# Kernel tuning notes

Hardware: AMD Instinct MI355X
Metric: run time of the kernel (lower is better)

## Reference

```python
import jax, jax.numpy as jnp
import numpy as np

N = 100000      # nodes
E = 320000      # edges
D = 128         # num_node_in_embeddings
DE = 256        # num_edge_in_embeddings = 2*D
NOBJ = 160
NREL = 27
BN_EPS = 1e-5   # eval-mode BatchNorm with running_mean=0, running_var=1


def setup_inputs() -> dict:
    key = jax.random.key(0)
    ks = jax.random.split(key, 24)
    f32 = jnp.float32
    def rn(k, shape, scale=0.05):
        return jax.random.normal(k, shape, f32) * scale
    return {
        "node_feats": jax.random.normal(ks[0], (N, D), f32),
        "edge_index": jax.random.randint(ks[1], (E, 2), 0, N),
        # GCNConv layers (W: [in,out], bias)
        "gcn1_W": rn(ks[2], (D, D // 2)), "gcn1_b": rn(ks[3], (D // 2,)),
        "gcn2_W": rn(ks[4], (D // 2, D)), "gcn2_b": rn(ks[5], (D,)),
        # edge attention (Linear(DE, D//2))
        "eattn_W": rn(ks[6], (DE, D // 2)), "eattn_b": rn(ks[7], (D // 2,)),
        # node attention (Linear(D, DE//2)) and indicator reduction (Linear(DE, DE//2))
        "nattn_W": rn(ks[8], (D, DE // 2)), "nattn_b": rn(ks[9], (DE // 2,)),
        "nred_W": rn(ks[10], (DE, DE // 2)), "nred_b": rn(ks[11], (DE // 2,)),
        # edge MLPs (1x1 Conv1d == Linear)
        "emlp1_W": rn(ks[12], (DE, DE // 2)), "emlp1_b": rn(ks[13], (DE // 2,)),
        "emlp2_W": rn(ks[14], (DE // 2, DE)), "emlp2_b": rn(ks[15], (DE,)),
        # node classification head
        "nlin1_W": rn(ks[16], (D, D // 2)),
        "nbn_g": jnp.ones((D // 2,), f32) + rn(ks[17], (D // 2,)),
        "nbn_b": rn(ks[18], (D // 2,)),
        "nlin2_W": rn(ks[19], (D // 2, NOBJ)),
        # edge classification head
        "elin1_W": rn(ks[20], (DE, DE // 2)),
        "ebn_g": jnp.ones((DE // 2,), f32) + rn(ks[21], (DE // 2,)),
        "ebn_b": rn(ks[22], (DE // 2,)),
        "elin2_W": rn(ks[23], (DE // 2, NREL)),
    }


def _seg_mean(vals, idx, n):
    # torch_scatter 'mean': sum / clamp(count, 1)
    s = jax.ops.segment_sum(vals, idx, num_segments=n)
    c = jax.ops.segment_sum(jnp.ones((vals.shape[0], 1), vals.dtype), idx, num_segments=n)
    return s / jnp.maximum(c, 1.0)


def _gcn_conv(x, src, dst, W, b, n):
    # PyG GCNConv, add_self_loops=True, symmetric normalization.
    lin = x @ W
    deg = jax.ops.segment_sum(jnp.ones((src.shape[0],), x.dtype), dst, num_segments=n) + 1.0
    dis = jax.lax.rsqrt(deg)                       # deg^{-1/2}, includes self-loop
    norm = dis[src] * dis[dst]                     # per-edge norm
    agg = jax.ops.segment_sum(lin[src] * norm[:, None], dst, num_segments=n)
    return agg + lin * (dis * dis)[:, None] + b    # self-loop term + bias


def _bn_eval(x, g, b):
    # eval-mode BatchNorm1d with running_mean=0, running_var=1
    return x * (g / jnp.sqrt(1.0 + BN_EPS)) + b


def reference(node_feats, edge_index, gcn1_W, gcn1_b, gcn2_W, gcn2_b,
              eattn_W, eattn_b, nattn_W, nattn_b, nred_W, nred_b,
              emlp1_W, emlp1_b, emlp2_W, emlp2_b,
              nlin1_W, nbn_g, nbn_b, nlin2_W,
              elin1_W, ebn_g, ebn_b, elin2_W):
    n = node_feats.shape[0]
    src = edge_index[:, 0]
    dst = edge_index[:, 1]

    # edge feature init: [subject, object - subject]  -> [E, DE]
    subj = node_feats[src]
    edge_feats = jnp.concatenate([subj, node_feats[dst] - subj], axis=1)

    # edge attention -> scatter-mean indicators over rows/cols -> node gate
    edge_ind = edge_feats @ eattn_W + eattn_b            # [E, D/2]
    row = _seg_mean(edge_ind, src, n)                    # [N, D/2]
    col = _seg_mean(edge_ind, dst, n)                    # [N, D/2]
    agg_edge_indicator = jax.nn.sigmoid(row * col)

    # two GCN layers (dropout is identity in eval mode)
    h = jax.nn.relu(_gcn_conv(node_feats, src, dst, gcn1_W, gcn1_b, n)) * agg_edge_indicator
    h = jax.nn.relu(_gcn_conv(h, src, dst, gcn2_W, gcn2_b, n))           # [N, D]

    # node attention -> per-edge gate
    node_ind = jax.nn.relu(h @ nattn_W + nattn_b)                        # [N, DE/2]
    econcat = jnp.concatenate([node_ind[src], node_ind[dst]], axis=1)    # [E, DE]
    agg_node_indicator = jax.nn.sigmoid(econcat @ nred_W + nred_b)       # [E, DE/2]

    # edge MLPs (1x1 convs == linears over edges)
    ef = jax.nn.relu(edge_feats @ emlp1_W + emlp1_b) * agg_node_indicator
    ef = jax.nn.relu(ef @ emlp2_W + emlp2_b)                             # [E, DE]

    # node head: linear -> BN(eval) -> leaky_relu(0.2) -> linear -> softmax over classes
    nx = jax.nn.leaky_relu(_bn_eval(h @ nlin1_W, nbn_g, nbn_b), 0.2)
    node_logits = jax.nn.softmax(nx @ nlin2_W, axis=1)                   # [N, NOBJ]

    # edge head: note original applies softmax on dim=1 of [1,E,NREL] -> over EDGES
    ex = jax.nn.leaky_relu(_bn_eval(ef @ elin1_W, ebn_g, ebn_b), 0.2)
    edge_logits = jax.nn.softmax(ex @ elin2_W, axis=0)                   # [E, NREL]

    return (node_logits, edge_logits)
```

## Files before the change

kernel.cpp:

```cpp
#include <hip/hip_runtime.h>

#define NN 100000
#define EE 320000

typedef unsigned int uint32;
typedef __attribute__((ext_vector_type(8))) short bf16x8;
typedef __attribute__((ext_vector_type(4))) float f32x4;
typedef __attribute__((ext_vector_type(16))) float f32x16;

__device__ __forceinline__ float4 ld4(const float* p){ return *(const float4*)p; }
__device__ __forceinline__ void st4(float* p, const float4 v){ *(float4*)p = v; }
__device__ __forceinline__ float sigm(float x){ return 1.f/(1.f + expf(-x)); }
__device__ __forceinline__ short f2b(float f){
  union { float f; uint32 u; } v; v.f = f;
  uint32 r = (v.u + 0x7FFFu + ((v.u>>16)&1u)) >> 16;
  return (short)r;
}
__device__ __forceinline__ float b2f(short s){
  union { uint32 u; float f; } v; v.u = ((uint32)(unsigned short)s) << 16; return v.f;
}

constexpr int EM_STORE=0, EM_BRELU=1, EM_BNLK=2;

template<int K,int NOUT,int EM>
__global__ __launch_bounds__(256) void gemm_k(
    const float* __restrict__ A,
    const float* __restrict__ W, const float* __restrict__ bias,
    const float* __restrict__ bng,
    float* __restrict__ C, int M)
{
  constexpr int CN = NOUT/16;
  __shared__ float As[16][68];
  __shared__ float Ws[16][NOUT];
  const int t  = threadIdx.x;
  const int tx = t & 15, ty = t >> 4;
  const int row0 = blockIdx.x * 64;

  float acc[4][CN];
  #pragma unroll
  for (int i=0;i<4;i++)
    #pragma unroll
    for (int j=0;j<CN;j++) acc[i][j]=0.f;

  const int r_st  = t >> 2;
  const int kq_st = (t & 3) * 4;

  for (int k0=0;k0<K;k0+=16) {
    {
      float4 v = make_float4(0.f,0.f,0.f,0.f);
      const int gr = row0 + r_st;
      if (gr < M) v = ld4(A + (size_t)gr*K + k0 + kq_st);
      As[kq_st+0][r_st]=v.x; As[kq_st+1][r_st]=v.y;
      As[kq_st+2][r_st]=v.z; As[kq_st+3][r_st]=v.w;
    }
    {
      constexpr int C4 = NOUT/4;
      for (int i=t;i<16*C4;i+=256){ int kk=i/C4, c4=(i%C4)*4;
        st4(&Ws[kk][c4], ld4(W + (size_t)(k0+kk)*NOUT + c4)); }
    }
    __syncthreads();
    #pragma unroll
    for (int kk=0;kk<16;kk++){
      float a0,a1,a2,a3;
      { const float4 av = *(const float4*)&As[kk][ty*4]; a0=av.x;a1=av.y;a2=av.z;a3=av.w; }
      float b[CN];
      if constexpr ((CN & 3) == 0) {
        #pragma unroll
        for (int j4=0;j4<CN;j4+=4){
          const float4 bv = *(const float4*)&Ws[kk][tx*CN+j4];
          b[j4]=bv.x;b[j4+1]=bv.y;b[j4+2]=bv.z;b[j4+3]=bv.w; }
      } else {
        #pragma unroll
        for (int j=0;j<CN;j++) b[j]=Ws[kk][tx*CN+j];
      }
      #pragma unroll
      for (int j=0;j<CN;j++){
        acc[0][j]=fmaf(a0,b[j],acc[0][j]);
        acc[1][j]=fmaf(a1,b[j],acc[1][j]);
        acc[2][j]=fmaf(a2,b[j],acc[2][j]);
        acc[3][j]=fmaf(a3,b[j],acc[3][j]);
      }
    }
    __syncthreads();
  }

  float sc[CN], sh[CN];
  if constexpr (EM==EM_BNLK) {
    const float r_ = rsqrtf(1.f + 1e-5f);
    #pragma unroll
    for (int j=0;j<CN;j++){ int c=tx*CN+j; sc[j]=bng[c]*r_; sh[j]=bias[c]; }
  }
  #pragma unroll
  for (int i=0;i<4;i++){
    const int r  = row0 + ty*4+i;
    if (r >= M) continue;
    #pragma unroll
    for (int j=0;j<CN;j++){
      const int c = tx*CN+j;
      float v = acc[i][j];
      if constexpr (EM==EM_BRELU) v = fmaxf(v + bias[c], 0.f);
      else if constexpr (EM==EM_BNLK){ float x = fmaf(v, sc[j], sh[j]); v = (x>0.f)? x : 0.2f*x; }
      C[(size_t)r*NOUT + c] = v;
    }
  }
}

__global__ void k_hist(const int* __restrict__ eidx, int* cntS, int* cntD, int E){
  int e = blockIdx.x*256+threadIdx.x; if (e>=E) return;
  atomicAdd(&cntS[eidx[2*e]], 1);
  atomicAdd(&cntD[eidx[2*e+1]], 1);
}
__global__ void k_scan_sum(const int* __restrict__ cnt, int* bsum, int n){
  __shared__ int red[256];
  const int b=blockIdx.x, t=threadIdx.x;
  int s=0;
  for (int i=b*1024+t; i<n && i<(b+1)*1024; i+=256) s += cnt[i];
  red[t]=s; __syncthreads();
  for (int o=128;o;o>>=1){ if(t<o) red[t]+=red[t+o]; __syncthreads(); }
  if (t==0) bsum[b]=red[0];
}
__global__ void k_scan_top(int* bsum, int nb){
  __shared__ int sh[256];
  const int t=threadIdx.x;
  int v=(t<nb)?bsum[t]:0;
  sh[t]=v; __syncthreads();
  for (int o=1;o<256;o<<=1){
    int u=0; if(t>=o) u=sh[t-o];
    __syncthreads();
    sh[t]+=u;
    __syncthreads();
  }
  if (t<nb) bsum[t]=sh[t]-v;
}
__global__ void k_scan_out(const int* __restrict__ cnt, const int* __restrict__ bofs,
                           int* __restrict__ off, int n){
  __shared__ int sh[256];
  const int b=blockIdx.x, t=threadIdx.x;
  const int base=b*1024+t*4;
  int c0=0,c1=0,c2=0,c3=0;
  if(base+0<n)c0=cnt[base+0];
  if(base+1<n)c1=cnt[base+1];
  if(base+2<n)c2=cnt[base+2];
  if(base+3<n)c3=cnt[base+3];
  int s=c0+c1+c2+c3;
  sh[t]=s; __syncthreads();
  int v=s;
  for (int o=1;o<256;o<<=1){
    int u=0; if(t>=o) u=sh[t-o];
    __syncthreads();
    sh[t]+=u;
    __syncthreads();
  }
  const int tofs = sh[t]-v + bofs[b];
  if(base+0<n) off[base+0]=tofs;
  if(base+1<n) off[base+1]=tofs+c0;
  if(base+2<n) off[base+2]=tofs+c0+c1;
  if(base+3<n) off[base+3]=tofs+c0+c1+c2;
}
__global__ void k_copyoff(const int* __restrict__ off, int* __restrict__ cur, int n){
  int i=blockIdx.x*256+threadIdx.x;
  if (i<n) cur[i]=off[i];
}
__global__ void k_setend(int* offS, int* offD, int n, int E){
  if (threadIdx.x==0 && blockIdx.x==0){ offS[n]=E; offD[n]=E; }
}
__global__ void k_fill(const int* __restrict__ eidx, int* curS, int* curD,
                       int* __restrict__ csrS, int* __restrict__ csrD, int E){
  int e=blockIdx.x*256+threadIdx.x; if (e>=E) return;
  const int s=eidx[2*e], d=eidx[2*e+1];
  csrS[atomicAdd(&curS[s],1)] = d;
  csrD[atomicAdd(&curD[d],1)] = s;
}
__global__ void k_dis(const int* __restrict__ cntD, float* __restrict__ dis, int n){
  int i=blockIdx.x*256+threadIdx.x; if(i>=n)return;
  dis[i]=rsqrtf((float)cntD[i]+1.f);
}

__global__ void k_wprep(const float* __restrict__ eattnW, const float* __restrict__ gcn1W,
                        float* __restrict__ Wcat){
  int idx=blockIdx.x*256+threadIdx.x; if (idx>=128*192) return;
  int k=idx/192, c=idx-k*192;
  float v;
  if (c<64)       v = eattnW[(size_t)(128+k)*64 + c];
  else if (c<128) v = eattnW[(size_t)k*64 + (c-64)] - eattnW[(size_t)(128+k)*64 + (c-64)];
  else            v = gcn1W[(size_t)k*64 + (c-128)];
  Wcat[idx]=v;
}

template<int NC>
__global__ void k_gather(const float* __restrict__ src, int stride, int colbase,
                         const int* __restrict__ off, const int* __restrict__ csr,
                         float* __restrict__ out, int n){
  constexpr int TPN = NC/4;
  const int t=threadIdx.x;
  const int node = blockIdx.x*(256/TPN) + t/TPN; if (node>=n) return;
  const int cq = (t%TPN)*4;
  const int j1=off[node+1];
  float4 acc = make_float4(0.f,0.f,0.f,0.f);
  for (int j=off[node]; j<j1; ++j){
    const float4 v = ld4(src + (size_t)csr[j]*stride + colbase + cq);
    acc.x+=v.x; acc.y+=v.y; acc.z+=v.z; acc.w+=v.w;
  }
  st4(out + (size_t)node*NC + cq, acc);
}

__global__ void k_aei3(const float* __restrict__ TUL, const float* __restrict__ Q,
                       const float* __restrict__ S, const int* __restrict__ cntS,
                       const int* __restrict__ cntD, const float* __restrict__ bias,
                       float* __restrict__ aei, int n){
  int idx=blockIdx.x*256+threadIdx.x; if (idx>=n*16) return;
  const int i=idx>>4, cq=(idx&15)*4;
  const float cS=(float)cntS[i], cD=(float)cntD[i];
  const float iS=1.f/fmaxf(cS,1.f), iD=1.f/fmaxf(cD,1.f);
  const float* tul = TUL + (size_t)i*192;
  const float4 T4=ld4(tul+cq), U4=ld4(tul+64+cq);
  const float4 Q4=ld4(Q+(size_t)i*64+cq), S4=ld4(S+(size_t)i*64+cq), b4=ld4(bias+cq);
  float4 o;
  o.x=sigm(((cS*(U4.x+b4.x)+Q4.x)*iS) * ((cD*(T4.x+b4.x)+S4.x)*iD));
  o.y=sigm(((cS*(U4.y+b4.y)+Q4.y)*iS) * ((cD*(T4.y+b4.y)+S4.y)*iD));
  o.z=sigm(((cS*(U4.z+b4.z)+Q4.z)*iS) * ((cD*(T4.z+b4.z)+S4.z)*iD));
  o.w=sigm(((cS*(U4.w+b4.w)+Q4.w)*iS) * ((cD*(T4.w+b4.w)+S4.w)*iD));
  st4(aei + (size_t)i*64 + cq, o);
}

template<int NC, bool AEI>
__global__ void k_gcnagg(const float* __restrict__ lin, int stride, int colbase,
                         const int* __restrict__ off, const int* __restrict__ csr,
                         const float* __restrict__ dis, const float* __restrict__ aei,
                         const float* __restrict__ bias, float* __restrict__ h, int n){
  constexpr int TPN = NC/4;
  const int t=threadIdx.x;
  const int node = blockIdx.x*(256/TPN) + t/TPN; if (node>=n) return;
  const int cq = (t%TPN)*4;
  const int j1=off[node+1];
  float4 acc = make_float4(0.f,0.f,0.f,0.f);
  for (int j=off[node]; j<j1; ++j){
    const int s=csr[j];
    const float w=dis[s];
    const float4 v = ld4(lin + (size_t)s*stride + colbase + cq);
    acc.x=fmaf(v.x,w,acc.x); acc.y=fmaf(v.y,w,acc.y);
    acc.z=fmaf(v.z,w,acc.z); acc.w=fmaf(v.w,w,acc.w);
  }
  const float dn=dis[node], d2=dn*dn;
  const float4 own=ld4(lin + (size_t)node*stride + colbase + cq), b4=ld4(bias+cq);
  float4 o;
  o.x=fmaxf(fmaf(acc.x,dn,fmaf(own.x,d2,b4.x)),0.f);
  o.y=fmaxf(fmaf(acc.y,dn,fmaf(own.y,d2,b4.y)),0.f);
  o.z=fmaxf(fmaf(acc.z,dn,fmaf(own.z,d2,b4.z)),0.f);
  o.w=fmaxf(fmaf(acc.w,dn,fmaf(own.w,d2,b4.w)),0.f);
  if (AEI){ const float4 m=ld4(aei+(size_t)node*NC+cq); o.x*=m.x;o.y*=m.y;o.z*=m.z;o.w*=m.w; }
  st4(h + (size_t)node*NC + cq, o);
}

__global__ void k_twtg(const float* __restrict__ Wa, const float* __restrict__ Wb,
                       short* __restrict__ Wt, int K, int N, int NP, int rowoff, int krot){
  int idx = blockIdx.x*256 + threadIdx.x;
  if (idx >= NP*K) return;
  int nn = idx / K, k = idx - nn*K;
  int ks = k + krot; if (ks >= K) ks -= K;
  float v = 0.f;
  if (nn < N){
    v = Wa[(size_t)(ks+rowoff)*N + nn];
    if (Wb) v -= Wb[(size_t)(ks+rowoff)*N + nn];
  }
  Wt[idx] = f2b(v);
}

template<int KSTRIDE, int NCOLTOT>
__device__ __forceinline__ void mm32(
    const short* __restrict__ Wt, int kbase,
    short (*As)[258], short (*Bs)[132],
    int t, int lane, int w, f32x16* acc)
{
  constexpr int NT = (NCOLTOT>=64)? NCOLTOT/64 : 1;
  const int lane31 = lane & 31, kh = lane >> 5;
  const int arow = (w>>1)*32 + lane31;
  const int colbase = (NCOLTOT>=64)? (w&1)*(NCOLTOT/2) : 0;
  {
    constexpr int PER = (NCOLTOT*16)/256;
    #pragma unroll
    for (int p=0;p<PER;p++){
      const int idx = t + p*256;
      const int col = idx >> 4, kq = idx & 15;
      *(float4*)&Bs[col][kq*8] = *(const float4*)(Wt + (size_t)col*KSTRIDE + kq*8);
    }
  }
  __syncthreads();
  #pragma unroll
  for (int ks=0; ks<8; ++ks){
    const bf16x8 a = *(const bf16x8*)&As[arow][kbase + ks*16 + kh*8];
    #pragma unroll
    for (int ct=0; ct<NT; ++ct){
      const bf16x8 b = *(const bf16x8*)&Bs[colbase + ct*32 + lane31][ks*16 + kh*8];
      acc[ct] = __builtin_amdgcn_mfma_f32_32x32x16_bf16(a, b, acc[ct], 0, 0, 0);
    }
  }
  __syncthreads();
}

__device__ __forceinline__ int rowof(int reg, int kh){
  return (reg & 3) + ((reg >> 2) << 3) + (kh << 2);
}

__global__ __launch_bounds__(256, 2) void k_pa(
  const float* __restrict__ niB, const float* __restrict__ nf,
  const short* __restrict__ wt_p1, const short* __restrict__ wt_p2,
  const short* __restrict__ wt_a1, const short* __restrict__ wt_a2,
  short* __restrict__ PAs, short* __restrict__ PAd, int n)
{
  __shared__ short As[64][258];
  __shared__ short Bs[128][132];
  short* OutS = &Bs[0][0];
  const int t = threadIdx.x, lane = t & 63, w = t >> 6;
  const int lane31 = lane & 31, kh = lane >> 5;
  const int n0 = blockIdx.x * 64;
  const int srow = t >> 2, q = t & 3;
  const int grow = n0 + srow;

#define STAGE_SRC(SRC)                                                       \
  {                                                                          \
    short* dst = &As[srow][q*32];                                            \
    if (grow < n){                                                           \
      const float* src = (SRC) + (size_t)grow*128 + q*32;                    \
      _Pragma("unroll")                                                      \
      for (int p=0;p<4;p++){                                                 \
        float4 u=ld4(src+p*8), v=ld4(src+p*8+4);                             \
        bf16x8 o;                                                            \
        o[0]=f2b(u.x);o[1]=f2b(u.y);o[2]=f2b(u.z);o[3]=f2b(u.w);             \
        o[4]=f2b(v.x);o[5]=f2b(v.y);o[6]=f2b(v.z);o[7]=f2b(v.w);             \
        *(bf16x8*)(dst+p*8)=o;                                               \
      }                                                                      \
    } else {                                                                 \
      _Pragma("unroll")                                                      \
      for (int p=0;p<4;p++) *(bf16x8*)(dst+p*8) = (bf16x8)0;                 \
    }                                                                        \
  }

#define OUT_AND_STORE(DST, CB)                                               \
  {                                                                          \
    const int colbase = (w&1)*64;                                            \
    _Pragma("unroll")                                                        \
    for (int ct=0;ct<2;ct++){                                                \
      _Pragma("unroll")                                                      \
      for (int reg=0;reg<16;reg++)                                           \
        OutS[((w>>1)*32 + rowof(reg,kh))*136 + colbase + ct*32 + lane31] =   \
            f2b(acc[ct][reg]);                                               \
    }                                                                        \
    __syncthreads();                                                         \
    if (grow < n){                                                           \
      const float* srcp = (const float*)&OutS[srow*136 + q*32];              \
      float* dstp = (float*)((DST) + (size_t)grow*256 + (CB) + q*32);        \
      _Pragma("unroll")                                                      \
      for (int p=0;p<4;p++) st4(dstp + p*4, ld4(srcp + p*4));                \
    }                                                                        \
    __syncthreads();                                                         \
  }

  f32x16 acc[2];
  STAGE_SRC(niB);
  acc[0]=(f32x16)(0.f); acc[1]=(f32x16)(0.f);
  mm32<128,128>(wt_p1, 0, As, Bs, t, lane, w, acc);
  OUT_AND_STORE(PAs, 0);
  acc[0]=(f32x16)(0.f); acc[1]=(f32x16)(0.f);
  mm32<128,128>(wt_p2, 0, As, Bs, t, lane, w, acc);
  OUT_AND_STORE(PAd, 0);
  STAGE_SRC(nf);
  acc[0]=(f32x16)(0.f); acc[1]=(f32x16)(0.f);
  mm32<128,128>(wt_a1, 0, As, Bs, t, lane, w, acc);
  OUT_AND_STORE(PAs, 128);
  acc[0]=(f32x16)(0.f); acc[1]=(f32x16)(0.f);
  mm32<128,128>(wt_a2, 0, As, Bs, t, lane, w, acc);
  OUT_AND_STORE(PAd, 128);
#undef STAGE_SRC
#undef OUT_AND_STORE
}

__global__ __launch_bounds__(256, 2) void k_edge(
  const short* __restrict__ PAs, const short* __restrict__ PAd,
  const int* __restrict__ eidx,
  const float* __restrict__ nredb, const float* __restrict__ e1b,
  const short* __restrict__ wt_e2, const float* __restrict__ e2b,
  const short* __restrict__ wt_l1, const float* __restrict__ ebng, const float* __restrict__ ebnb,
  const short* __restrict__ wt_l2,
  float* __restrict__ elog)
{
  __shared__ short As[64][258];
  __shared__ short Bs[128][132];
  const int t = threadIdx.x, lane = t & 63, w = t >> 6;
  const int lane31 = lane & 31, kh = lane >> 5;
  const int row0 = blockIdx.x * 64;

  {
    const int srow = t >> 2, q = t & 3;
    const int e = row0 + srow;
    const int s = eidx[2*e], d = eidx[2*e+1];
    const short* ps = PAs + (size_t)s*256;
    const short* pd = PAd + (size_t)d*256;
    #pragma unroll
    for (int c0=0;c0<32;c0+=8){
      const int c = q*32 + c0;
      const bf16x8 p1 = *(const bf16x8*)(ps + c);
      const bf16x8 p2 = *(const bf16x8*)(pd + c);
      const bf16x8 a1 = *(const bf16x8*)(ps + 128 + c);
      const bf16x8 a2 = *(const bf16x8*)(pd + 128 + c);
      const float4 bg0=ld4(nredb+c), bg1=ld4(nredb+c+4);
      const float4 be0=ld4(e1b+c),   be1=ld4(e1b+c+4);
      const float bg[8]={bg0.x,bg0.y,bg0.z,bg0.w,bg1.x,bg1.y,bg1.z,bg1.w};
      const float be[8]={be0.x,be0.y,be0.z,be0.w,be1.x,be1.y,be1.z,be1.w};
      bf16x8 o;
      #pragma unroll
      for (int j=0;j<8;j++){
        const float g = sigm(b2f(p1[j]) + b2f(p2[j]) + bg[j]);
        const float v = fmaxf(b2f(a1[j]) + b2f(a2[j]) + be[j], 0.f) * g;
        o[j] = f2b(v);
      }
      *(bf16x8*)&As[srow][c] = o;
    }
  }

  f32x16 acc[2];
  acc[0]=(f32x16)(0.f); acc[1]=(f32x16)(0.f);
  mm32<128,128>(wt_e2, 0, As, Bs, t, lane, w, acc);
  #pragma unroll
  for (int ct=0;ct<2;ct++){
    const int col = (w&1)*64 + ct*32 + lane31;
    const float bb = e2b[col];
    #pragma unroll
    for (int reg=0;reg<16;reg++)
      As[(w>>1)*32 + rowof(reg,kh)][128+col] = f2b(fmaxf(acc[ct][reg] + bb, 0.f));
  }
  acc[0]=(f32x16)(0.f); acc[1]=(f32x16)(0.f);
  mm32<128,128>(wt_e2 + (size_t)128*128, 0, As, Bs, t, lane, w, acc);
  #pragma unroll
  for (int ct=0;ct<2;ct++){
    const int col = (w&1)*64 + ct*32 + lane31;
    const float bb = e2b[128+col];
    #pragma unroll
    for (int reg=0;reg<16;reg++)
      As[(w>>1)*32 + rowof(reg,kh)][col] = f2b(fmaxf(acc[ct][reg] + bb, 0.f));
  }

  acc[0]=(f32x16)(0.f); acc[1]=(f32x16)(0.f);
  mm32<256,128>(wt_l1,       0,   As, Bs, t, lane, w, acc);
  mm32<256,128>(wt_l1 + 128, 128, As, Bs, t, lane, w, acc);
  {
    const float r_ = rsqrtf(1.f + 1e-5f);
    #pragma unroll
    for (int ct=0;ct<2;ct++){
      const int col = (w&1)*64 + ct*32 + lane31;
      const float sc = ebng[col]*r_, sh = ebnb[col];
      #pragma unroll
      for (int reg=0;reg<16;reg++){
        const float x = fmaf(acc[ct][reg], sc, sh);
        As[(w>>1)*32 + rowof(reg,kh)][col] = f2b((x>0.f)? x : 0.2f*x);
      }
    }
  }

  f32x16 acc5 = (f32x16)(0.f);
  mm32<128,32>(wt_l2, 0, As, Bs, t, lane, w, &acc5);

  float* Lb = (float*)&As[0][0];
  if ((w&1)==0 && lane31 < 27){
    #pragma unroll
    for (int reg=0;reg<16;reg++)
      Lb[((w>>1)*32 + rowof(reg,kh))*28 + lane31] = acc5[reg];
  }
  __syncthreads();
  for (int i=t; i<64*27; i+=256){
    int rr = i/27, cc = i - rr*27;
    elog[(size_t)(row0+rr)*27 + cc] = Lb[rr*28 + cc];
  }
}

__global__ __launch_bounds__(256) void k_softmax_row(float* __restrict__ x, int M){
  const int wave = threadIdx.x>>6, lane = threadIdx.x&63;
  const int r = blockIdx.x*4 + wave; if (r>=M) return;
  float* p = x + (size_t)r*160;
  float v0 = p[lane], v1 = p[64+lane];
  float v2 = (lane<32)? p[128+lane] : -3.4e38f;
  float m = fmaxf(fmaxf(v0,v1),v2);
  for (int o=32;o;o>>=1) m = fmaxf(m, __shfl_xor(m,o));
  float e0=expf(v0-m), e1=expf(v1-m), e2=(lane<32)?expf(v2-m):0.f;
  float s=e0+e1+e2;
  for (int o=32;o;o>>=1) s += __shfl_xor(s,o);
  float inv = 1.f/s;
  p[lane]=e0*inv; p[64+lane]=e1*inv; if(lane<32)p[128+lane]=e2*inv;
}
__global__ void k_colmax(const float* __restrict__ x, uint32* __restrict__ cmax_u, int E){
  __shared__ float red[8][32];
  const int t=threadIdx.x, col=t&31, seg=t>>5;
  float m = -3.4e38f;
  if (col < 27)
    for (int r = blockIdx.x*8 + seg; r < E; r += gridDim.x*8)
      m = fmaxf(m, x[(size_t)r*27+col]);
  red[seg][col]=m; __syncthreads();
  if (t<32){
    float mm=red[0][t];
    #pragma unroll
    for (int s2=1;s2<8;s2++) mm=fmaxf(mm,red[s2][t]);
    if (t<27){
      uint32 u=__float_as_uint(mm);
      u = (u&0x80000000u)? ~u : (u|0x80000000u);
      atomicMax(&cmax_u[t], u);
    }
  }
}
__global__ void k_colfix(const uint32* __restrict__ cmax_u, float* __restrict__ cmaxf){
  int t=threadIdx.x; if (t>=27) return;
  uint32 u=cmax_u[t];
  cmaxf[t] = (u&0x80000000u)? __uint_as_float(u&0x7FFFFFFFu) : __uint_as_float(~u);
}
__global__ void k_colsum(const float* __restrict__ x, const float* __restrict__ cmaxf,
                         float* __restrict__ csum, int E){
  __shared__ float red[8][32];
  const int t=threadIdx.x, col=t&31, seg=t>>5;
  float s = 0.f;
  if (col < 27){
    const float cm = cmaxf[col];
    for (int r = blockIdx.x*8 + seg; r < E; r += gridDim.x*8)
      s += expf(x[(size_t)r*27+col] - cm);
  }
  red[seg][col]=s; __syncthreads();
  if (t<32){
    float ss=red[0][t];
    #pragma unroll
    for (int s2=1;s2<8;s2++) ss+=red[s2][t];
    if (t<27) atomicAdd(&csum[t], ss);
  }
}
__global__ void k_colnorm(float* __restrict__ x, const float* __restrict__ cmaxf,
                          const float* __restrict__ csum, int E){
  int idx=blockIdx.x*256+threadIdx.x;
  if (idx >= E*27) return;
  int c = idx - (idx/27)*27;
  x[idx] = expf(x[idx]-cmaxf[c]) / csum[c];
}

extern "C" void kernel_launch(void* const* d_in, const int* in_sizes, int n_in,
                              void* d_out, int out_size, void* d_ws, size_t ws_size,
                              hipStream_t stream)
{
  const float* nf     = (const float*)d_in[0];
  const int*   eidx   = (const int*)  d_in[1];
  const float* gcn1W  = (const float*)d_in[2];
  const float* gcn1b  = (const float*)d_in[3];
  const float* gcn2W  = (const float*)d_in[4];
  const float* gcn2b  = (const float*)d_in[5];
  const float* eattnW = (const float*)d_in[6];
  const float* eattnb = (const float*)d_in[7];
  const float* nattnW = (const float*)d_in[8];
  const float* nattnb = (const float*)d_in[9];
  const float* nredW  = (const float*)d_in[10];
  const float* nredb  = (const float*)d_in[11];
  const float* emlp1W = (const float*)d_in[12];
  const float* emlp1b = (const float*)d_in[13];
  const float* emlp2W = (const float*)d_in[14];
  const float* emlp2b = (const float*)d_in[15];
  const float* nlin1W = (const float*)d_in[16];
  const float* nbng   = (const float*)d_in[17];
  const float* nbnb   = (const float*)d_in[18];
  const float* nlin2W = (const float*)d_in[19];
  const float* elin1W = (const float*)d_in[20];
  const float* ebng   = (const float*)d_in[21];
  const float* ebnb   = (const float*)d_in[22];
  const float* elin2W = (const float*)d_in[23];
  (void)in_sizes; (void)n_in; (void)out_size; (void)ws_size;

  const int N = NN, E = EE;
  float* out  = (float*)d_out;
  float* nlog = out;
  float* elog = out + (size_t)N*160;

  float* ws   = (float*)d_ws;
  float* h2   = ws;
  float* lin2 = ws + (size_t)N*128;
  float* Q    = lin2;
  float* S    = lin2 + (size_t)N*64;
  float* niB  = lin2;
  float* nx   = lin2;
  float* TUL  = ws + (size_t)N*256;
  float* h1   = ws + (size_t)N*448;
  short* PAs  = (short*)TUL;
  short* PAd  = PAs + (size_t)N*256;
  float* aei  = ws + (size_t)N*512;
  float* dis  = ws + (size_t)N*576;
  float* smalls = ws + (size_t)N*577;
  float* Wcat = smalls + 128;
  int*   ip   = (int*)(Wcat + 24576);
  int* cntS = ip;
  int* cntD = ip + N;
  int* offS = ip + 2*N;
  int* offD = ip + 3*N + 64;
  int* curS = ip + 4*N + 128;
  int* curD = ip + 5*N + 128;
  int* csrS = ip + 6*N + 128;
  int* csrD = ip + 6*N + 128 + E;
  int* bsum = ip + 6*N + 128 + 2*E;
  short* wtb  = (short*)(bsum + 256);
  short* wt_p1 = wtb;
  short* wt_p2 = wtb + 16384;
  short* wt_a1 = wtb + 32768;
  short* wt_a2 = wtb + 49152;
  short* wt_e2 = wtb + 65536;
  short* wt_l1 = wtb + 98304;
  short* wt_l2 = wtb + 131072;

  const int NB1024 = (N + 1023)/1024;

  k_twtg<<<64, 256,0,stream>>>(nredW,  nullptr, wt_p1, 128,128,128, 0,   0);
  k_twtg<<<64, 256,0,stream>>>(nredW,  nullptr, wt_p2, 128,128,128, 128, 0);
  k_twtg<<<64, 256,0,stream>>>(emlp1W, emlp1W+(size_t)128*128, wt_a1, 128,128,128, 0, 0);
  k_twtg<<<64, 256,0,stream>>>(emlp1W, nullptr, wt_a2, 128,128,128, 128, 0);
  k_twtg<<<128,256,0,stream>>>(emlp2W, nullptr, wt_e2, 128,256,256, 0,   0);
  k_twtg<<<128,256,0,stream>>>(elin1W, nullptr, wt_l1, 256,128,128, 0, 128);
  k_twtg<<<16, 256,0,stream>>>(elin2W, nullptr, wt_l2, 128,27, 32,  0,   0);
  k_wprep<<<96,256,0,stream>>>(eattnW, gcn1W, Wcat);

  (void)hipMemsetAsync(cntS, 0, 2*(size_t)N*sizeof(int), stream);
  k_hist<<<(E+255)/256,256,0,stream>>>(eidx, cntS, cntD, E);
  k_scan_sum<<<NB1024,256,0,stream>>>(cntS, bsum, N);
  k_scan_top<<<1,256,0,stream>>>(bsum, NB1024);
  k_scan_out<<<NB1024,256,0,stream>>>(cntS, bsum, offS, N);
  k_scan_sum<<<NB1024,256,0,stream>>>(cntD, bsum, N);
  k_scan_top<<<1,256,0,stream>>>(bsum, NB1024);
  k_scan_out<<<NB1024,256,0,stream>>>(cntD, bsum, offD, N);
  k_setend<<<1,64,0,stream>>>(offS, offD, N, E);
  k_copyoff<<<(N+255)/256,256,0,stream>>>(offS, curS, N);
  k_copyoff<<<(N+255)/256,256,0,stream>>>(offD, curD, N);
  k_fill<<<(E+255)/256,256,0,stream>>>(eidx, curS, curD, csrS, csrD, E);
  k_dis<<<(N+255)/256,256,0,stream>>>(cntD, dis, N);

  gemm_k<128,192,EM_STORE><<<(N+63)/64,256,0,stream>>>(nf, Wcat, nullptr, nullptr, TUL, N);

  k_gather<64><<<(N+15)/16,256,0,stream>>>(TUL, 192, 0,  offS, csrS, Q, N);
  k_gather<64><<<(N+15)/16,256,0,stream>>>(TUL, 192, 64, offD, csrD, S, N);
  k_aei3<<<(N*16+255)/256,256,0,stream>>>(TUL, Q, S, cntS, cntD, eattnb, aei, N);

  k_gcnagg<64,true><<<(N+15)/16,256,0,stream>>>(TUL, 192, 128, offD, csrD, dis, aei, gcn1b, h1, N);

  gemm_k<64,128,EM_STORE><<<(N+63)/64,256,0,stream>>>(h1, gcn2W, nullptr, nullptr, lin2, N);
  k_gcnagg<128,false><<<(N+7)/8,256,0,stream>>>(lin2, 128, 0, offD, csrD, dis, nullptr, gcn2b, h2, N);

  gemm_k<128,128,EM_BRELU><<<(N+63)/64,256,0,stream>>>(h2, nattnW, nattnb, nullptr, niB, N);

  k_pa<<<(N+63)/64,256,0,stream>>>(niB, nf, wt_p1, wt_p2, wt_a1, wt_a2, PAs, PAd, N);

  k_edge<<<E/64,256,0,stream>>>(
      PAs, PAd, eidx,
      nredb, emlp1b, wt_e2, emlp2b,
      wt_l1, ebng, ebnb, wt_l2, elog);

  gemm_k<128,64,EM_BNLK><<<(N+63)/64,256,0,stream>>>(h2, nlin1W, nbnb, nbng, nx, N);
  gemm_k<64,160,EM_STORE><<<(N+63)/64,256,0,stream>>>(nx, nlin2W, nullptr, nullptr, nlog, N);
  k_softmax_row<<<(N+3)/4,256,0,stream>>>(nlog, N);

  (void)hipMemsetAsync(smalls, 0, 96*sizeof(float), stream);
  k_colmax<<<1024,256,0,stream>>>(elog, (uint32*)smalls, E);
  k_colfix<<<1,32,0,stream>>>((const uint32*)smalls, smalls+64);
  k_colsum<<<1024,256,0,stream>>>(elog, smalls+64, smalls+32, E);
  k_colnorm<<<(E*27+255)/256,256,0,stream>>>(elog, smalls+64, smalls+32, E);
}
```

Before: 1.022 ms.

## Fuse neighbor gathers, attention gate and GCN1 aggregation; fold node-attn GEMM into projection kernel

Merges the two neighbor-sum gathers, the edge-attention sigmoid kernel and the first GCN aggregation into one kernel that walks each node's source and destination CSR lists once, so the Q, S and aei intermediates are never written to global memory. The node-attention linear+ReLU is computed inside the projection kernel with MFMA, and its bf16 result is kept in shared memory instead of being round-tripped through global memory. The scan kernel now also writes the cursor array, which removes the separate copy kernels. In exchange the fused kernels carry more registers and shared-memory pressure, and the bf16 rounding of the attention output happens at a different point.

```diff
diff --git a/kernel.cpp b/kernel.cpp
--- a/kernel.cpp
+++ b/kernel.cpp
@@ -133,7 +133,7 @@
   if (t<nb) bsum[t]=sh[t]-v;
 }
 __global__ void k_scan_out(const int* __restrict__ cnt, const int* __restrict__ bofs,
-                           int* __restrict__ off, int n){
+                           int* __restrict__ off, int* __restrict__ cur, int n){
   __shared__ int sh[256];
   const int b=blockIdx.x, t=threadIdx.x;
   const int base=b*1024+t*4;
@@ -152,14 +152,10 @@
     __syncthreads();
   }
   const int tofs = sh[t]-v + bofs[b];
-  if(base+0<n) off[base+0]=tofs;
-  if(base+1<n) off[base+1]=tofs+c0;
-  if(base+2<n) off[base+2]=tofs+c0+c1;
-  if(base+3<n) off[base+3]=tofs+c0+c1+c2;
-}
-__global__ void k_copyoff(const int* __restrict__ off, int* __restrict__ cur, int n){
-  int i=blockIdx.x*256+threadIdx.x;
-  if (i<n) cur[i]=off[i];
+  if(base+0<n){ off[base+0]=tofs;          cur[base+0]=tofs; }
+  if(base+1<n){ off[base+1]=tofs+c0;       cur[base+1]=tofs+c0; }
+  if(base+2<n){ off[base+2]=tofs+c0+c1;    cur[base+2]=tofs+c0+c1; }
+  if(base+3<n){ off[base+3]=tofs+c0+c1+c2; cur[base+3]=tofs+c0+c1+c2; }
 }
 __global__ void k_setend(int* offS, int* offD, int n, int E){
   if (threadIdx.x==0 && blockIdx.x==0){ offS[n]=E; offD[n]=E; }
@@ -187,40 +183,59 @@
   Wcat[idx]=v;
 }
 
-template<int NC>
-__global__ void k_gather(const float* __restrict__ src, int stride, int colbase,
-                         const int* __restrict__ off, const int* __restrict__ csr,
-                         float* __restrict__ out, int n){
-  constexpr int TPN = NC/4;
-  const int t=threadIdx.x;
-  const int node = blockIdx.x*(256/TPN) + t/TPN; if (node>=n) return;
-  const int cq = (t%TPN)*4;
-  const int j1=off[node+1];
-  float4 acc = make_float4(0.f,0.f,0.f,0.f);
-  for (int j=off[node]; j<j1; ++j){
-    const float4 v = ld4(src + (size_t)csr[j]*stride + colbase + cq);
-    acc.x+=v.x; acc.y+=v.y; acc.z+=v.z; acc.w+=v.w;
-  }
-  st4(out + (size_t)node*NC + cq, acc);
-}
-
-__global__ void k_aei3(const float* __restrict__ TUL, const float* __restrict__ Q,
-                       const float* __restrict__ S, const int* __restrict__ cntS,
-                       const int* __restrict__ cntD, const float* __restrict__ bias,
-                       float* __restrict__ aei, int n){
-  int idx=blockIdx.x*256+threadIdx.x; if (idx>=n*16) return;
-  const int i=idx>>4, cq=(idx&15)*4;
-  const float cS=(float)cntS[i], cD=(float)cntD[i];
+__global__ __launch_bounds__(256) void k_fuse1(
+    const float* __restrict__ TUL,
+    const int* __restrict__ offS, const int* __restrict__ csrS,
+    const int* __restrict__ offD, const int* __restrict__ csrD,
+    const int* __restrict__ cntS, const int* __restrict__ cntD,
+    const float* __restrict__ dis,
+    const float* __restrict__ eattnb, const float* __restrict__ gcn1b,
+    float* __restrict__ h1, int n)
+{
+  const int t = threadIdx.x;
+  const int node = blockIdx.x*16 + (t>>4); if (node>=n) return;
+  const int cq = (t&15)*4;
+
+  float4 Q = make_float4(0.f,0.f,0.f,0.f);
+  {
+    const int j1 = offS[node+1];
+    for (int j=offS[node]; j<j1; ++j){
+      const float4 v = ld4(TUL + (size_t)csrS[j]*192 + cq);
+      Q.x+=v.x; Q.y+=v.y; Q.z+=v.z; Q.w+=v.w;
+    }
+  }
+  float4 S = make_float4(0.f,0.f,0.f,0.f);
+  float4 AG = make_float4(0.f,0.f,0.f,0.f);
+  {
+    const int j1 = offD[node+1];
+    for (int j=offD[node]; j<j1; ++j){
+      const int s = csrD[j];
+      const float wgt = dis[s];
+      const float* bp = TUL + (size_t)s*192;
+      const float4 u = ld4(bp + 64 + cq);
+      const float4 L = ld4(bp + 128 + cq);
+      S.x+=u.x; S.y+=u.y; S.z+=u.z; S.w+=u.w;
+      AG.x=fmaf(L.x,wgt,AG.x); AG.y=fmaf(L.y,wgt,AG.y);
+      AG.z=fmaf(L.z,wgt,AG.z); AG.w=fmaf(L.w,wgt,AG.w);
+    }
+  }
+  const float cS=(float)cntS[node], cD=(float)cntD[node];
   const float iS=1.f/fmaxf(cS,1.f), iD=1.f/fmaxf(cD,1.f);
-  const float* tul = TUL + (size_t)i*192;
-  const float4 T4=ld4(tul+cq), U4=ld4(tul+64+cq);
-  const float4 Q4=ld4(Q+(size_t)i*64+cq), S4=ld4(S+(size_t)i*64+cq), b4=ld4(bias+cq);
-  float4 o;
-  o.x=sigm(((cS*(U4.x+b4.x)+Q4.x)*iS) * ((cD*(T4.x+b4.x)+S4.x)*iD));
-  o.y=sigm(((cS*(U4.y+b4.y)+Q4.y)*iS) * ((cD*(T4.y+b4.y)+S4.y)*iD));
-  o.z=sigm(((cS*(U4.z+b4.z)+Q4.z)*iS) * ((cD*(T4.z+b4.z)+S4.z)*iD));
-  o.w=sigm(((cS*(U4.w+b4.w)+Q4.w)*iS) * ((cD*(T4.w+b4.w)+S4.w)*iD));
-  st4(aei + (size_t)i*64 + cq, o);
+  const float* own = TUL + (size_t)node*192;
+  const float4 T4=ld4(own+cq), U4=ld4(own+64+cq), L4=ld4(own+128+cq);
+  const float4 b4=ld4(eattnb+cq), g4=ld4(gcn1b+cq);
+  float4 aei;
+  aei.x = sigm(((cS*(U4.x+b4.x)+Q.x)*iS) * ((cD*(T4.x+b4.x)+S.x)*iD));
+  aei.y = sigm(((cS*(U4.y+b4.y)+Q.y)*iS) * ((cD*(T4.y+b4.y)+S.y)*iD));
+  aei.z = sigm(((cS*(U4.z+b4.z)+Q.z)*iS) * ((cD*(T4.z+b4.z)+S.z)*iD));
+  aei.w = sigm(((cS*(U4.w+b4.w)+Q.w)*iS) * ((cD*(T4.w+b4.w)+S.w)*iD));
+  const float dn=dis[node], d2=dn*dn;
+  float4 h;
+  h.x = fmaxf(fmaf(AG.x,dn,fmaf(L4.x,d2,g4.x)),0.f)*aei.x;
+  h.y = fmaxf(fmaf(AG.y,dn,fmaf(L4.y,d2,g4.y)),0.f)*aei.y;
+  h.z = fmaxf(fmaf(AG.z,dn,fmaf(L4.z,d2,g4.z)),0.f)*aei.z;
+  h.w = fmaxf(fmaf(AG.w,dn,fmaf(L4.w,d2,g4.w)),0.f)*aei.w;
+  st4(h1 + (size_t)node*64 + cq, h);
 }
 
 template<int NC, bool AEI>
@@ -302,8 +317,10 @@
   return (reg & 3) + ((reg >> 2) << 3) + (kh << 2);
 }
 
-__global__ __launch_bounds__(256, 2) void k_pa(
-  const float* __restrict__ niB, const float* __restrict__ nf,
+__global__ __launch_bounds__(256, 2) void k_pa2(
+  const float* __restrict__ h2, const float* __restrict__ nf,
+  const float* __restrict__ nattnb,
+  const short* __restrict__ wt_na,
   const short* __restrict__ wt_p1, const short* __restrict__ wt_p2,
   const short* __restrict__ wt_a1, const short* __restrict__ wt_a2,
   short* __restrict__ PAs, short* __restrict__ PAd, int n)
@@ -357,12 +374,22 @@
   }
 
   f32x16 acc[2];
-  STAGE_SRC(niB);
-  acc[0]=(f32x16)(0.f); acc[1]=(f32x16)(0.f);
-  mm32<128,128>(wt_p1, 0, As, Bs, t, lane, w, acc);
+  STAGE_SRC(h2);
+  acc[0]=(f32x16)(0.f); acc[1]=(f32x16)(0.f);
+  mm32<128,128>(wt_na, 0, As, Bs, t, lane, w, acc);
+  #pragma unroll
+  for (int ct=0;ct<2;ct++){
+    const int col = (w&1)*64 + ct*32 + lane31;
+    const float bb = nattnb[col];
+    #pragma unroll
+    for (int reg=0;reg<16;reg++)
+      As[(w>>1)*32 + rowof(reg,kh)][128+col] = f2b(fmaxf(acc[ct][reg] + bb, 0.f));
+  }
+  acc[0]=(f32x16)(0.f); acc[1]=(f32x16)(0.f);
+  mm32<128,128>(wt_p1, 128, As, Bs, t, lane, w, acc);
   OUT_AND_STORE(PAs, 0);
   acc[0]=(f32x16)(0.f); acc[1]=(f32x16)(0.f);
-  mm32<128,128>(wt_p2, 0, As, Bs, t, lane, w, acc);
+  mm32<128,128>(wt_p2, 128, As, Bs, t, lane, w, acc);
   OUT_AND_STORE(PAd, 0);
   STAGE_SRC(nf);
   acc[0]=(f32x16)(0.f); acc[1]=(f32x16)(0.f);
@@ -575,15 +602,11 @@
   float* ws   = (float*)d_ws;
   float* h2   = ws;
   float* lin2 = ws + (size_t)N*128;
-  float* Q    = lin2;
-  float* S    = lin2 + (size_t)N*64;
-  float* niB  = lin2;
   float* nx   = lin2;
   float* TUL  = ws + (size_t)N*256;
   float* h1   = ws + (size_t)N*448;
   short* PAs  = (short*)TUL;
   short* PAd  = PAs + (size_t)N*256;
-  float* aei  = ws + (size_t)N*512;
   float* dis  = ws + (size_t)N*576;
   float* smalls = ws + (size_t)N*577;
   float* Wcat = smalls + 128;
@@ -605,6 +628,7 @@
   short* wt_e2 = wtb + 65536;
   short* wt_l1 = wtb + 98304;
   short* wt_l2 = wtb + 131072;
+  short* wt_na = wtb + 135168;
 
   const int NB1024 = (N + 1023)/1024;
 
@@ -615,36 +639,31 @@
   k_twtg<<<128,256,0,stream>>>(emlp2W, nullptr, wt_e2, 128,256,256, 0,   0);
   k_twtg<<<128,256,0,stream>>>(elin1W, nullptr, wt_l1, 256,128,128, 0, 128);
   k_twtg<<<16, 256,0,stream>>>(elin2W, nullptr, wt_l2, 128,27, 32,  0,   0);
+  k_twtg<<<64, 256,0,stream>>>(nattnW, nullptr, wt_na, 128,128,128, 0,   0);
   k_wprep<<<96,256,0,stream>>>(eattnW, gcn1W, Wcat);
 
   (void)hipMemsetAsync(cntS, 0, 2*(size_t)N*sizeof(int), stream);
   k_hist<<<(E+255)/256,256,0,stream>>>(eidx, cntS, cntD, E);
   k_scan_sum<<<NB1024,256,0,stream>>>(cntS, bsum, N);
   k_scan_top<<<1,256,0,stream>>>(bsum, NB1024);
-  k_scan_out<<<NB1024,256,0,stream>>>(cntS, bsum, offS, N);
+  k_scan_out<<<NB1024,256,0,stream>>>(cntS, bsum, offS, curS, N);
   k_scan_sum<<<NB1024,256,0,stream>>>(cntD, bsum, N);
   k_scan_top<<<1,256,0,stream>>>(bsum, NB1024);
-  k_scan_out<<<NB1024,256,0,stream>>>(cntD, bsum, offD, N);
+  k_scan_out<<<NB1024,256,0,stream>>>(cntD, bsum, offD, curD, N);
   k_setend<<<1,64,0,stream>>>(offS, offD, N, E);
-  k_copyoff<<<(N+255)/256,256,0,stream>>>(offS, curS, N);
-  k_copyoff<<<(N+255)/256,256,0,stream>>>(offD, curD, N);
   k_fill<<<(E+255)/256,256,0,stream>>>(eidx, curS, curD, csrS, csrD, E);
   k_dis<<<(N+255)/256,256,0,stream>>>(cntD, dis, N);
 
   gemm_k<128,192,EM_STORE><<<(N+63)/64,256,0,stream>>>(nf, Wcat, nullptr, nullptr, TUL, N);
 
-  k_gather<64><<<(N+15)/16,256,0,stream>>>(TUL, 192, 0,  offS, csrS, Q, N);
-  k_gather<64><<<(N+15)/16,256,0,stream>>>(TUL, 192, 64, offD, csrD, S, N);
-  k_aei3<<<(N*16+255)/256,256,0,stream>>>(TUL, Q, S, cntS, cntD, eattnb, aei, N);
-
-  k_gcnagg<64,true><<<(N+15)/16,256,0,stream>>>(TUL, 192, 128, offD, csrD, dis, aei, gcn1b, h1, N);
+  k_fuse1<<<(N+15)/16,256,0,stream>>>(TUL, offS, csrS, offD, csrD,
+      cntS, cntD, dis, eattnb, gcn1b, h1, N);
 
   gemm_k<64,128,EM_STORE><<<(N+63)/64,256,0,stream>>>(h1, gcn2W, nullptr, nullptr, lin2, N);
   k_gcnagg<128,false><<<(N+7)/8,256,0,stream>>>(lin2, 128, 0, offD, csrD, dis, nullptr, gcn2b, h2, N);
 
-  gemm_k<128,128,EM_BRELU><<<(N+63)/64,256,0,stream>>>(h2, nattnW, nattnb, nullptr, niB, N);
-
-  k_pa<<<(N+63)/64,256,0,stream>>>(niB, nf, wt_p1, wt_p2, wt_a1, wt_a2, PAs, PAd, N);
+  k_pa2<<<(N+63)/64,256,0,stream>>>(h2, nf, nattnb, wt_na,
+      wt_p1, wt_p2, wt_a1, wt_a2, PAs, PAd, N);
 
   k_edge<<<E/64,256,0,stream>>>(
       PAs, PAd, eidx,
```

Measured after the change: 959.0 us. 1.07x faster.
